# Kernel optimization log

Hardware: AMD Instinct MI355X
Metric: run time of the kernel (lower is better)

Reference implementation:

```python
import jax, jax.numpy as jnp
import numpy as np

# Production-scale dims (see shape_source)
B, C, H, W = 4, 128, 64, 64
RADIUS = 0.2
TEMP = 0.1
PAD_VALUE = 0.0
P = int(H * RADIUS) * 2 + 1  # local window size kH = kW = 25


def setup_inputs() -> dict:
    key = jax.random.key(0)
    k1, k2 = jax.random.split(key)
    query = jax.random.normal(k1, (B, C, H, W), dtype=jnp.float32)
    keys = jax.random.normal(k2, (B, C, H, W), dtype=jnp.float32)
    return {"query": query, "keys": keys}


def _make_idx_map(h_dim, w_dim, p):
    # Equivalent of F.unfold(arange(H*W).view(H,W), kernel=(P,P), pad=P//2).clamp(min=0)
    # idx[h, w, p1, p2] = linear index of (h+p1-P//2, w+p2-P//2), 0 if out of bounds
    off = np.arange(p) - p // 2
    hh = np.arange(h_dim)[:, None, None, None] + off[None, None, :, None]  # (H,1,P,1)
    ww = np.arange(w_dim)[None, :, None, None] + off[None, None, None, :]  # (1,W,1,P)
    valid = (hh >= 0) & (hh < h_dim) & (ww >= 0) & (ww < w_dim)
    idx = np.where(valid, hh * w_dim + ww, 0)  # (H,W,P,P)
    return jnp.asarray(idx.reshape(h_dim * w_dim, p * p), dtype=jnp.int32)

_IDX_MAP = _make_idx_map(H, W, P)  # (H*W, P*P) int32 constant


def _local_correlation(query, keys, p):
    # spatial_correlation_sample(kernel=1, patch=P, stride=1, pad=0, dilation=1):
    # att[b,p1,p2,h,w] = sum_c query[b,c,h,w] * keys_zero_padded[b,c,h+p1-P//2,w+p2-P//2]
    pad = p // 2
    keys_pad = jnp.pad(keys, ((0, 0), (0, 0), (pad, pad), (pad, pad)))

    def corr_one(i):
        p1, p2 = i // p, i % p
        k = jax.lax.dynamic_slice(keys_pad, (0, 0, p1, p2), keys.shape)
        return jnp.einsum('bchw,bchw->bhw', query, k)

    att = jax.lax.map(corr_one, jnp.arange(p * p))  # (P*P, B, H, W); sequential keeps memory low
    return jnp.transpose(att, (1, 2, 3, 0))  # b h w (p1 p2)


def reference(query, keys):
    n_pix = H * W
    att = _local_correlation(query, keys, P) / TEMP  # (B,H,W,P*P)
    # knn(): pad_value==0, topk==0 -> mask exact zeros (out-of-window zero-padded corrs) to -10
    A = jnp.where(att == PAD_VALUE, jnp.float32(-10.0), att)
    A = jnp.exp(A.reshape(B, n_pix, P * P))  # b (h w) n
    # scatter_add into dense (B, H*W, H*W) affinity map
    q_idx = jnp.arange(n_pix)[:, None]  # (HW,1)
    out = jnp.zeros((B, n_pix, n_pix), dtype=A.dtype)
    out = out.at[:, q_idx, _IDX_MAP].add(A)
    # rearr 'b (h w) n -> b n h w'
    return out.reshape(B, H, W, n_pix).transpose(0, 3, 1, 2)
```

## Files before the change

### kernel.cpp

```cpp
#include <hip/hip_runtime.h>
#include <math.h>


#define BDIM 256
constexpr int Bn = 4, Cc = 128, Hh = 64, Ww = 64, HW = 4096;
constexpr int P = 25, Rr = 12, T = 8;

__device__ __forceinline__ int cntf(int x) {
    int c = P;
    if (x < Rr) c -= (Rr - x);
    if (x > (Hh - 1 - Rr)) c -= (x - (Hh - 1 - Rr));
    return c;
}

__global__ __launch_bounds__(BDIM) void localwalk_kernel(
    const float* __restrict__ query, const float* __restrict__ keys,
    float* __restrict__ out)
{
    const int jt = blockIdx.x;
    const int jh = blockIdx.y;
    const int b  = blockIdx.z;
    const int jw0 = jt * T;
    const int t = threadIdx.x;

    __shared__ float S[T * P * P];

    const float E10 = expf(-10.0f);
    const bool special = (jh == 0) && (jt == 0);

    const float* kb = keys + (size_t)b * Cc * HW + jh * Ww + jw0;
    for (int i = t; i < Cc * T; i += BDIM)
        S[i] = kb[(size_t)(i >> 3) * HW + (i & 7)];
    __syncthreads();

    const int wloc = t & 31, hs = t >> 5;
    const int w = jw0 - Rr + wloc;
    const int wa = min(max(w, 0), Ww - 1);
    const bool wvalid = (w >= 0) && (w < Ww);

    int ha[4]; bool hv[4];
    #pragma unroll
    for (int r = 0; r < 4; ++r) {
        int hloc = hs + 8 * r;
        int h = jh - Rr + hloc;
        hv[r] = (hloc < P) && (h >= 0) && (h < Hh);
        ha[r] = min(max(h, 0), Hh - 1);
    }

    float acc[4][T];
    #pragma unroll
    for (int r = 0; r < 4; ++r)
        #pragma unroll
        for (int jj = 0; jj < T; ++jj) acc[r][jj] = 0.f;

    const float* qb = query + (size_t)b * Cc * HW;
    int qoff[4];
    #pragma unroll
    for (int r = 0; r < 4; ++r) qoff[r] = ha[r] * Ww + wa;

    #pragma unroll 4
    for (int c = 0; c < Cc; ++c) {
        const float* qc = qb + (size_t)c * HW;
        float qv[4];
        #pragma unroll
        for (int r = 0; r < 4; ++r) qv[r] = qc[qoff[r]];
        float4 k0 = *(const float4*)&S[c * 8];
        float4 k1 = *(const float4*)&S[c * 8 + 4];
        float kk[T] = {k0.x, k0.y, k0.z, k0.w, k1.x, k1.y, k1.z, k1.w};
        #pragma unroll
        for (int jj = 0; jj < T; ++jj)
            #pragma unroll
            for (int r = 0; r < 4; ++r)
                acc[r][jj] = fmaf(qv[r], kk[jj], acc[r][jj]);
    }

    __syncthreads();

    #pragma unroll
    for (int jj = 0; jj < T; ++jj) {
        const int d = wloc - jj;
        const bool dv = (d >= 0) && (d < P) && wvalid;
        #pragma unroll
        for (int r = 0; r < 4; ++r) {
            if (!dv || !hv[r]) continue;
            float att = acc[r][jj] / 0.1f;
            if (att == 0.0f) att = -10.0f;
            att = fminf(att, 88.0f);
            S[(jj * P + (hs + 8 * r)) * P + d] = expf(att);
        }
    }
    __syncthreads();

    float4* orow4 = (float4*)(out + ((size_t)(b * HW + jh * Ww + jw0)) * HW);
    for (int k = 0; k < 32; ++k) {
        int fi = t + k * BDIM;
        int jj  = fi >> 10;
        int idx = fi & 1023;
        int h   = idx >> 4;
        int w4  = (idx & 15) * 4;
        int hl  = h - (jh - Rr);
        bool hin = (hl >= 0) && (hl < P);

        float4 v = make_float4(0.f, 0.f, 0.f, 0.f);
        if (special && jj == 0) {
            int ch = cntf(h);
            v.x = (float)(P * P - ch * cntf(w4 + 0)) * E10;
            v.y = (float)(P * P - ch * cntf(w4 + 1)) * E10;
            v.z = (float)(P * P - ch * cntf(w4 + 2)) * E10;
            v.w = (float)(P * P - ch * cntf(w4 + 3)) * E10;
        }
        if (hin) {
            int base = (jj * P + hl) * P;
            int off  = jw0 + jj - Rr;
            int we0  = w4 - off;
            if ((unsigned)(we0 + 0) < (unsigned)P) v.x += S[base + we0 + 0];
            if ((unsigned)(we0 + 1) < (unsigned)P) v.y += S[base + we0 + 1];
            if ((unsigned)(we0 + 2) < (unsigned)P) v.z += S[base + we0 + 2];
            if ((unsigned)(we0 + 3) < (unsigned)P) v.w += S[base + we0 + 3];
        }
        orow4[fi] = v;
    }
}

extern "C" void kernel_launch(void* const* d_in, const int* in_sizes, int n_in,
                              void* d_out, int out_size, void* d_ws, size_t ws_size,
                              hipStream_t stream) {
    const float* query = (const float*)d_in[0];
    const float* keys  = (const float*)d_in[1];
    float* out = (float*)d_out;
    dim3 grid(Ww / T, Hh, Bn);
    localwalk_kernel<<<grid, dim3(BDIM), 0, stream>>>(query, keys, out);
}
```

Measured before the change: 380.9 us.

## Split dense output fill into separate kernel and scatter window values afterwards

Splits the work into two kernels. The first streams the full dense output with zeros plus the special boundary row. The second computes the correlations and writes only the in-window exp values straight to global memory, so the shared-memory staging of the window tile is no longer needed. The intent is a simpler, purely bandwidth-bound fill and a lighter compute kernel. The cost is a second launch and scattered, non-coalesced extra writes to locations the fill has already written.

```diff
diff --git a/kernel.cpp b/kernel.cpp
--- a/kernel.cpp
+++ b/kernel.cpp
@@ -5,6 +5,7 @@
 #define BDIM 256
 constexpr int Bn = 4, Cc = 128, Hh = 64, Ww = 64, HW = 4096;
 constexpr int P = 25, Rr = 12, T = 8;
+constexpr size_t OUT_ELEMS = (size_t)Bn * HW * HW;
 
 __device__ __forceinline__ int cntf(int x) {
     int c = P;
@@ -13,7 +14,29 @@
     return c;
 }
 
-__global__ __launch_bounds__(BDIM) void localwalk_kernel(
+__global__ __launch_bounds__(BDIM) void localwalk_fill(float* __restrict__ out) {
+    const float E10 = expf(-10.0f);
+    const size_t nt  = (size_t)gridDim.x * BDIM;
+    const size_t tid = (size_t)blockIdx.x * BDIM + threadIdx.x;
+    float4* o4 = (float4*)out;
+    const size_t n4 = OUT_ELEMS / 4;
+    for (size_t i = tid; i < n4; i += nt) {
+        float4 v = make_float4(0.f, 0.f, 0.f, 0.f);
+        size_t e0 = i * 4;
+        if ((e0 & (size_t)(HW * HW - 1)) < (size_t)HW) {
+            int hw = (int)(e0 & (size_t)(HW - 1));
+            int h = hw >> 6, w0 = hw & 63;
+            int ch = cntf(h);
+            v.x = (float)(P * P - ch * cntf(w0 + 0)) * E10;
+            v.y = (float)(P * P - ch * cntf(w0 + 1)) * E10;
+            v.z = (float)(P * P - ch * cntf(w0 + 2)) * E10;
+            v.w = (float)(P * P - ch * cntf(w0 + 3)) * E10;
+        }
+        o4[i] = v;
+    }
+}
+
+__global__ __launch_bounds__(BDIM) void localwalk_compute(
     const float* __restrict__ query, const float* __restrict__ keys,
     float* __restrict__ out)
 {
@@ -23,7 +46,7 @@
     const int jw0 = jt * T;
     const int t = threadIdx.x;
 
-    __shared__ float S[T * P * P];
+    __shared__ float S[Cc * T];
 
     const float E10 = expf(-10.0f);
     const bool special = (jh == 0) && (jt == 0);
@@ -74,51 +97,24 @@
                 acc[r][jj] = fmaf(qv[r], kk[jj], acc[r][jj]);
     }
 
-    __syncthreads();
-
     #pragma unroll
     for (int jj = 0; jj < T; ++jj) {
         const int d = wloc - jj;
         const bool dv = (d >= 0) && (d < P) && wvalid;
+        float* obase = out + ((size_t)(b * HW + jh * Ww + jw0 + jj)) * HW;
+        const bool isj0 = special && (jj == 0);
         #pragma unroll
         for (int r = 0; r < 4; ++r) {
             if (!dv || !hv[r]) continue;
+            const int h = ha[r];
             float att = acc[r][jj] / 0.1f;
             if (att == 0.0f) att = -10.0f;
             att = fminf(att, 88.0f);
-            S[(jj * P + (hs + 8 * r)) * P + d] = expf(att);
+            float e = expf(att);
+            if (isj0)
+                e += (float)(P * P - cntf(h) * cntf(w)) * E10;
+            obase[h * Ww + w] = e;
         }
-    }
-    __syncthreads();
-
-    float4* orow4 = (float4*)(out + ((size_t)(b * HW + jh * Ww + jw0)) * HW);
-    for (int k = 0; k < 32; ++k) {
-        int fi = t + k * BDIM;
-        int jj  = fi >> 10;
-        int idx = fi & 1023;
-        int h   = idx >> 4;
-        int w4  = (idx & 15) * 4;
-        int hl  = h - (jh - Rr);
-        bool hin = (hl >= 0) && (hl < P);
-
-        float4 v = make_float4(0.f, 0.f, 0.f, 0.f);
-        if (special && jj == 0) {
-            int ch = cntf(h);
-            v.x = (float)(P * P - ch * cntf(w4 + 0)) * E10;
-            v.y = (float)(P * P - ch * cntf(w4 + 1)) * E10;
-            v.z = (float)(P * P - ch * cntf(w4 + 2)) * E10;
-            v.w = (float)(P * P - ch * cntf(w4 + 3)) * E10;
-        }
-        if (hin) {
-            int base = (jj * P + hl) * P;
-            int off  = jw0 + jj - Rr;
-            int we0  = w4 - off;
-            if ((unsigned)(we0 + 0) < (unsigned)P) v.x += S[base + we0 + 0];
-            if ((unsigned)(we0 + 1) < (unsigned)P) v.y += S[base + we0 + 1];
-            if ((unsigned)(we0 + 2) < (unsigned)P) v.z += S[base + we0 + 2];
-            if ((unsigned)(we0 + 3) < (unsigned)P) v.w += S[base + we0 + 3];
-        }
-        orow4[fi] = v;
     }
 }
 
@@ -128,6 +124,7 @@
     const float* query = (const float*)d_in[0];
     const float* keys  = (const float*)d_in[1];
     float* out = (float*)d_out;
+    localwalk_fill<<<2048, BDIM, 0, stream>>>(out);
     dim3 grid(Ww / T, Hh, Bn);
-    localwalk_kernel<<<grid, dim3(BDIM), 0, stream>>>(query, keys, out);
+    localwalk_compute<<<grid, dim3(BDIM), 0, stream>>>(query, keys, out);
 }
```

New measurement: 404.4 us. 6.2% more time.

## Write window results directly from registers and zero-fill only outside window

Applied to the files above, without the earlier changes.

Remaps threads so each one computes four adjacent w positions with a single float4 query load, then writes the exp-masked window values straight to global memory from registers. The shared-memory staging of the P*P window per output row and its two extra barriers are removed. The zero-fill pass now skips float4 columns covered by the direct window writes. This cuts shared memory use and the extra shared-memory round trip, but makes the write pattern less uniform and spreads the window and zero stores across two loops.

```diff
diff --git a/kernel.cpp b/kernel.cpp
--- a/kernel.cpp
+++ b/kernel.cpp
@@ -13,7 +13,14 @@
     return c;
 }
 
-__global__ __launch_bounds__(BDIM) void localwalk_kernel(
+__device__ __forceinline__ float expmask(float a) {
+    float att = a / 0.1f;
+    if (att == 0.0f) att = -10.0f;
+    att = fminf(att, 88.0f);
+    return expf(att);
+}
+
+__global__ __launch_bounds__(BDIM) void localwalk_fused(
     const float* __restrict__ query, const float* __restrict__ keys,
     float* __restrict__ out)
 {
@@ -23,7 +30,7 @@
     const int jw0 = jt * T;
     const int t = threadIdx.x;
 
-    __shared__ float S[T * P * P];
+    __shared__ float S[Cc * T];
 
     const float E10 = expf(-10.0f);
     const bool special = (jh == 0) && (jt == 0);
@@ -33,92 +40,82 @@
         S[i] = kb[(size_t)(i >> 3) * HW + (i & 7)];
     __syncthreads();
 
-    const int wloc = t & 31, hs = t >> 5;
-    const int w = jw0 - Rr + wloc;
-    const int wa = min(max(w, 0), Ww - 1);
-    const bool wvalid = (w >= 0) && (w < Ww);
-
-    int ha[4]; bool hv[4];
-    #pragma unroll
-    for (int r = 0; r < 4; ++r) {
-        int hloc = hs + 8 * r;
-        int h = jh - Rr + hloc;
-        hv[r] = (hloc < P) && (h >= 0) && (h < Hh);
-        ha[r] = min(max(h, 0), Hh - 1);
-    }
+    const int hs = t >> 3;
+    const int wg = t & 7;
+    const int h  = jh - Rr + hs;
+    const int w0 = jw0 - Rr + 4 * wg;
+    const bool hvalid = (h >= 0) && (h < Hh);
+    const bool hwin   = hvalid && (hs < P);
+    const bool wgood  = (w0 >= 0) && (w0 + 3 < Ww);
+    const int  haddr  = min(max(h, 0), Hh - 1);
+    const int  w0addr = wgood ? w0 : 0;
 
     float acc[4][T];
     #pragma unroll
-    for (int r = 0; r < 4; ++r)
+    for (int k = 0; k < 4; ++k)
         #pragma unroll
-        for (int jj = 0; jj < T; ++jj) acc[r][jj] = 0.f;
+        for (int jj = 0; jj < T; ++jj) acc[k][jj] = 0.f;
 
-    const float* qb = query + (size_t)b * Cc * HW;
-    int qoff[4];
-    #pragma unroll
-    for (int r = 0; r < 4; ++r) qoff[r] = ha[r] * Ww + wa;
+    const float* qp = query + (size_t)b * Cc * HW + haddr * Ww + w0addr;
 
     #pragma unroll 4
     for (int c = 0; c < Cc; ++c) {
-        const float* qc = qb + (size_t)c * HW;
-        float qv[4];
-        #pragma unroll
-        for (int r = 0; r < 4; ++r) qv[r] = qc[qoff[r]];
+        float4 q  = *(const float4*)(qp + (size_t)c * HW);
         float4 k0 = *(const float4*)&S[c * 8];
         float4 k1 = *(const float4*)&S[c * 8 + 4];
         float kk[T] = {k0.x, k0.y, k0.z, k0.w, k1.x, k1.y, k1.z, k1.w};
+        float qq[4] = {q.x, q.y, q.z, q.w};
         #pragma unroll
         for (int jj = 0; jj < T; ++jj)
             #pragma unroll
-            for (int r = 0; r < 4; ++r)
-                acc[r][jj] = fmaf(qv[r], kk[jj], acc[r][jj]);
+            for (int k = 0; k < 4; ++k)
+                acc[k][jj] = fmaf(qq[k], kk[jj], acc[k][jj]);
     }
 
-    __syncthreads();
-
-    #pragma unroll
-    for (int jj = 0; jj < T; ++jj) {
-        const int d = wloc - jj;
-        const bool dv = (d >= 0) && (d < P) && wvalid;
+    if (hvalid && wgood) {
+        float* drow = out + ((size_t)(b * HW + jh * Ww + jw0)) * HW + h * Ww + w0;
         #pragma unroll
-        for (int r = 0; r < 4; ++r) {
-            if (!dv || !hv[r]) continue;
-            float att = acc[r][jj] / 0.1f;
-            if (att == 0.0f) att = -10.0f;
-            att = fminf(att, 88.0f);
-            S[(jj * P + (hs + 8 * r)) * P + d] = expf(att);
+        for (int jj = 0; jj < T; ++jj) {
+            float4 v = make_float4(0.f, 0.f, 0.f, 0.f);
+            const int jw = jw0 + jj;
+            if (hwin) {
+                #pragma unroll
+                for (int k = 0; k < 4; ++k) {
+                    int d = w0 + k - jw;
+                    if (d >= -Rr && d <= Rr)
+                        ((float*)&v)[k] = expmask(acc[k][jj]);
+                }
+            }
+            if (special && jj == 0) {
+                int ch = cntf(h);
+                v.x += (float)(P * P - ch * cntf(w0 + 0)) * E10;
+                v.y += (float)(P * P - ch * cntf(w0 + 1)) * E10;
+                v.z += (float)(P * P - ch * cntf(w0 + 2)) * E10;
+                v.w += (float)(P * P - ch * cntf(w0 + 3)) * E10;
+            }
+            *(float4*)(drow + (size_t)jj * HW) = v;
         }
     }
-    __syncthreads();
 
-    float4* orow4 = (float4*)(out + ((size_t)(b * HW + jh * Ww + jw0)) * HW);
+    const int h0 = max(0, jh - Rr), h1 = min(Hh - 1, jh + 19);
+    const int c0 = max(0, jw0 - Rr) >> 2, c1 = min(Ww - 4, jw0 + 16) >> 2;
+    float4* strip4 = (float4*)(out + ((size_t)(b * HW + jh * Ww + jw0)) * HW);
     for (int k = 0; k < 32; ++k) {
-        int fi = t + k * BDIM;
+        int fi  = t + k * BDIM;
         int jj  = fi >> 10;
         int idx = fi & 1023;
-        int h   = idx >> 4;
-        int w4  = (idx & 15) * 4;
-        int hl  = h - (jh - Rr);
-        bool hin = (hl >= 0) && (hl < P);
-
+        int hE  = idx >> 4;
+        int cE  = idx & 15;
+        if (hE >= h0 && hE <= h1 && cE >= c0 && cE <= c1) continue;
         float4 v = make_float4(0.f, 0.f, 0.f, 0.f);
         if (special && jj == 0) {
-            int ch = cntf(h);
-            v.x = (float)(P * P - ch * cntf(w4 + 0)) * E10;
-            v.y = (float)(P * P - ch * cntf(w4 + 1)) * E10;
-            v.z = (float)(P * P - ch * cntf(w4 + 2)) * E10;
-            v.w = (float)(P * P - ch * cntf(w4 + 3)) * E10;
+            int ch = cntf(hE), wE = cE * 4;
+            v.x = (float)(P * P - ch * cntf(wE + 0)) * E10;
+            v.y = (float)(P * P - ch * cntf(wE + 1)) * E10;
+            v.z = (float)(P * P - ch * cntf(wE + 2)) * E10;
+            v.w = (float)(P * P - ch * cntf(wE + 3)) * E10;
         }
-        if (hin) {
-            int base = (jj * P + hl) * P;
-            int off  = jw0 + jj - Rr;
-            int we0  = w4 - off;
-            if ((unsigned)(we0 + 0) < (unsigned)P) v.x += S[base + we0 + 0];
-            if ((unsigned)(we0 + 1) < (unsigned)P) v.y += S[base + we0 + 1];
-            if ((unsigned)(we0 + 2) < (unsigned)P) v.z += S[base + we0 + 2];
-            if ((unsigned)(we0 + 3) < (unsigned)P) v.w += S[base + we0 + 3];
-        }
-        orow4[fi] = v;
+        strip4[fi] = v;
     }
 }
 
@@ -129,5 +126,5 @@
     const float* keys  = (const float*)d_in[1];
     float* out = (float*)d_out;
     dim3 grid(Ww / T, Hh, Bn);
-    localwalk_kernel<<<grid, dim3(BDIM), 0, stream>>>(query, keys, out);
+    localwalk_fused<<<grid, dim3(BDIM), 0, stream>>>(query, keys, out);
 }
```

Result: slower. 395.2 us (+3.7%).
